# Performance work log

Hardware: AMD Instinct MI355X
Metric: run time of the kernel (lower is better)

The kernel has to match this reference:

```python
import jax, jax.numpy as jnp
import numpy as np

H = 51  # hidden size hard-coded in the module

def _lstm_cell(x_t, h, c, W_ih, W_hh, b_ih, b_hh):
    # PyTorch LSTMCell gate order: i, f, g, o
    gates = x_t @ W_ih.T + b_ih + h @ W_hh.T + b_hh  # [B, 4H]
    i, f, g, o = jnp.split(gates, 4, axis=-1)
    c_new = jax.nn.sigmoid(f) * c + jax.nn.sigmoid(i) * jnp.tanh(g)
    h_new = jax.nn.sigmoid(o) * jnp.tanh(c_new)
    return h_new, c_new


def setup_inputs() -> dict:
    key = jax.random.key(0)
    ks = jax.random.split(key, 11)
    B, T = 4096, 1024
    s = 1.0 / np.sqrt(H)
    return {
        "x": jax.random.normal(ks[0], (B, T), jnp.float32),
        "W_ih1": jax.random.uniform(ks[1], (4 * H, 1), jnp.float32, -s, s),
        "W_hh1": jax.random.uniform(ks[2], (4 * H, H), jnp.float32, -s, s),
        "b_ih1": jax.random.uniform(ks[3], (4 * H,), jnp.float32, -s, s),
        "b_hh1": jax.random.uniform(ks[4], (4 * H,), jnp.float32, -s, s),
        "W_ih2": jax.random.uniform(ks[5], (4 * H, H), jnp.float32, -s, s),
        "W_hh2": jax.random.uniform(ks[6], (4 * H, H), jnp.float32, -s, s),
        "b_ih2": jax.random.uniform(ks[7], (4 * H,), jnp.float32, -s, s),
        "b_hh2": jax.random.uniform(ks[8], (4 * H,), jnp.float32, -s, s),
        "W_lin": jax.random.uniform(ks[9], (1, H), jnp.float32, -s, s),
        "b_lin": jax.random.uniform(ks[10], (1,), jnp.float32, -s, s),
        "future": 64,
    }


def reference(x, W_ih1, W_hh1, b_ih1, b_hh1, W_ih2, W_hh2, b_ih2, b_hh2, W_lin, b_lin, future):
    B = x.shape[0]
    zeros = jnp.zeros((B, H), x.dtype)

    def step(carry, x_t):
        h1, c1, h2, c2 = carry
        h1, c1 = _lstm_cell(x_t, h1, c1, W_ih1, W_hh1, b_ih1, b_hh1)
        h2, c2 = _lstm_cell(h1, h2, c2, W_ih2, W_hh2, b_ih2, b_hh2)
        out = h2 @ W_lin.T + b_lin  # [B, 1]
        return (h1, c1, h2, c2), out

    xs = x.T[:, :, None]  # [T, B, 1]
    carry, outs = jax.lax.scan(step, (zeros, zeros, zeros, zeros), xs)

    def fut_step(carry, _):
        (h1, c1, h2, c2), out = carry
        h1, c1 = _lstm_cell(out, h1, c1, W_ih1, W_hh1, b_ih1, b_hh1)
        h2, c2 = _lstm_cell(h1, h2, c2, W_ih2, W_hh2, b_ih2, b_hh2)
        out = h2 @ W_lin.T + b_lin
        return ((h1, c1, h2, c2), out), out

    if future > 0:
        last_out = outs[-1]
        _, fut_outs = jax.lax.scan(fut_step, (carry, last_out), None, length=future)
        outs = jnp.concatenate([outs, fut_outs], axis=0)  # [T+future, B, 1]

    return outs[:, :, 0].T  # [B, T+future]
```

## Files before the change

kernel.cpp:

```cpp
#include <hip/hip_runtime.h>

#define HH    51
#define T_SEQ 1024
#define T_TOT 1088
#define B_TOT 4096
#define MT    16
#define NTH   512

typedef __attribute__((ext_vector_type(8))) short bf8_t;
typedef __attribute__((ext_vector_type(4))) float f32x4;

#define H1H_O 0
#define H1L_O 4096
#define H2H_O 8192
#define H2L_O 12288
#define XB_O  16384
#define OB_O  18432
#define PT_O  20480
#define SM_SZ 20992

#define L2E 1.44269504088896f

#if __has_builtin(__builtin_amdgcn_exp2f)
#define FEXP2 __builtin_amdgcn_exp2f
#else
#define FEXP2 exp2f
#endif
#if __has_builtin(__builtin_amdgcn_rcpf)
#define FRCP __builtin_amdgcn_rcpf
#else
#define FRCP(v) (1.f / (v))
#endif

__device__ __forceinline__ short f2bf(float f) {
  unsigned u = __builtin_bit_cast(unsigned, f);
  u += 0x7fffu + ((u >> 16) & 1u);
  return (short)(u >> 16);
}
__device__ __forceinline__ float bf2f(short s) {
  unsigned u = ((unsigned)(unsigned short)s) << 16;
  return __builtin_bit_cast(float, u);
}
__device__ __forceinline__ float lsig(float v) { return FRCP(1.f + FEXP2(v)); }

__device__ __forceinline__ f32x4 MFMA(bf8_t a, bf8_t b, f32x4 c) {
  return __builtin_amdgcn_mfma_f32_16x16x32_bf16(a, b, c, 0, 0, 0);
}
__device__ __forceinline__ bf8_t ldA(const char* base, int row, int off) {
  off ^= ((row & 7) << 4);
  return *reinterpret_cast<const bf8_t*>(base + row * 128 + off);
}
__device__ __forceinline__ void sthl(char* WH, char* WL, int row, int boff, float v) {
  const int o = row * 128 + (boff ^ ((row & 7) << 4));
  const unsigned u = __builtin_bit_cast(unsigned, v);
  *reinterpret_cast<short*>(WH + o) = (short)(u >> 16);
  const float rem = v - __builtin_bit_cast(float, u & 0xffff0000u);
  *reinterpret_cast<short*>(WL + o) = (short)(__builtin_bit_cast(unsigned, rem) >> 16);
}

__global__ __launch_bounds__(NTH, 1)
void lstm_mfma_kernel(const float* __restrict__ x,
                      const float* __restrict__ Wih1, const float* __restrict__ Whh1,
                      const float* __restrict__ bih1, const float* __restrict__ bhh1,
                      const float* __restrict__ Wih2, const float* __restrict__ Whh2,
                      const float* __restrict__ bih2, const float* __restrict__ bhh2,
                      const float* __restrict__ Wlin, const float* __restrict__ blin,
                      float* __restrict__ out)
{
  extern __shared__ char smc[];
  float* smf = (float*)smc;
  const int tid  = threadIdx.x;
  const int lane = tid & 63;
  const int w    = tid >> 6;
  const int cl   = lane & 15;
  const int gr   = lane >> 4;
  const int rng  = w & 3;
  const bool isL2 = (w >= 4);
  const int jo   = rng * 16 + cl;
  const bool jv  = (jo < HH);
  const int bg0  = blockIdx.x * MT;

  for (int i = tid; i < SM_SZ / 4; i += NTH) smf[i] = 0.f;

  const float gsc[4] = {-L2E, -L2E, 2.f * L2E, -L2E};

  bf8_t Bh[4][4], Bl[4][4];
  #pragma unroll
  for (int g = 0; g < 4; ++g) {
    #pragma unroll
    for (int kb = 0; kb < 4; ++kb) {
      bf8_t vh, vl;
      const bool dead = (!isL2 && kb >= 2);
      const float* Wsrc = isL2 ? (kb < 2 ? Wih2 : Whh2) : Whh1;
      const int kbase = (kb & 1) * 32;
      #pragma unroll
      for (int s = 0; s < 8; ++s) {
        const int ku = kbase + gr * 8 + s;
        float v = (!dead && jv && ku < HH) ? Wsrc[(g * HH + jo) * HH + ku] * gsc[g] : 0.f;
        if (!isL2 && kb == 1 && ku == 53) v = jv ? Wih1[g * HH + jo] * gsc[g] : 0.f;
        const short hh = f2bf(v);
        vh[s] = hh;
        vl[s] = f2bf(v - bf2f(hh));
      }
      Bh[g][kb] = vh; Bl[g][kb] = vl;
    }
  }
  bf8_t Bo[2];
  #pragma unroll
  for (int kb = 0; kb < 2; ++kb) {
    bf8_t v;
    #pragma unroll
    for (int s = 0; s < 8; ++s) {
      const int ku = kb * 32 + gr * 8 + s;
      float wv = (ku < HH) ? Wlin[ku] : 0.f;
      const short hh = f2bf(wv);
      v[s] = (cl == 0) ? hh : (cl == 1) ? f2bf(wv - bf2f(hh)) : (short)0;
    }
    Bo[kb] = v;
  }
  float cbv[4], wih1v[4];
  #pragma unroll
  for (int g = 0; g < 4; ++g) {
    cbv[g]   = jv ? (isL2 ? (bih2[g*HH+jo] + bhh2[g*HH+jo])
                          : (bih1[g*HH+jo] + bhh1[g*HH+jo])) * gsc[g] : 0.f;
    wih1v[g] = (jv && !isL2) ? Wih1[g*HH+jo] * gsc[g] : 0.f;
  }
  const float wlv = (jv && isL2) ? Wlin[jo] : 0.f;
  const float bl  = blin[0];
  float cst[4] = {0.f, 0.f, 0.f, 0.f};

  auto act_h = [&](const f32x4 acc[4], int r) -> float {
    const float si = lsig(acc[0][r]);
    const float sf = lsig(acc[1][r]);
    const float tg = 1.f - 2.f * lsig(acc[2][r]);
    const float so = lsig(acc[3][r]);
    const float cn = sf * cst[r] + si * tg;
    cst[r] = cn;
    return so * (1.f - 2.f * lsig(cn * (2.f * L2E)));
  };

  auto writeOB = [&](int tw, const float ov[4]) {
    if (cl == 0) {
      const int po = (tw >> 4) & 1, cc = tw & 15;
      #pragma unroll
      for (int r = 0; r < 4; ++r)
        smf[OB_O/4 + po*256 + (gr*4 + r)*16 + cc] = ov[r];
    }
  };

  auto do_l1 = [&](const int p, const float* xv, const int t) {
    const char* RH = smc + H1H_O + (p ^ 1) * 2048;
    const char* RL = smc + H1L_O + (p ^ 1) * 2048;
    bf8_t a0 = ldA(RH, cl, gr*16), a1 = ldA(RH, cl, 64 + gr*16);
    bf8_t l0 = ldA(RL, cl, gr*16), l1 = ldA(RL, cl, 64 + gr*16);
    f32x4 acc[4];
    __builtin_amdgcn_s_setprio(1);
    #pragma unroll
    for (int g = 0; g < 4; ++g) {
      f32x4 a = {cbv[g], cbv[g], cbv[g], cbv[g]};
      a = MFMA(a0, Bh[g][0], a); a = MFMA(a1, Bh[g][1], a);
      a = MFMA(l0, Bh[g][0], a); a = MFMA(l1, Bh[g][1], a);
      a = MFMA(a0, Bl[g][0], a); a = MFMA(a1, Bl[g][1], a);
      acc[g] = a;
    }
    __builtin_amdgcn_s_setprio(0);
    if (xv) {
      #pragma unroll
      for (int g = 0; g < 4; ++g)
        #pragma unroll
        for (int r = 0; r < 4; ++r) acc[g][r] += wih1v[g] * xv[r];
    }
    char* WH = smc + H1H_O + p * 2048;
    char* WL = smc + H1L_O + p * 2048;
    #pragma unroll
    for (int r = 0; r < 4; ++r) {
      const float hv = act_h(acc, r);
      if (jv) sthl(WH, WL, gr * 4 + r, 2 * jo, hv);
    }
    if (!xv && rng == 3 && (t + 1) < T_SEQ) {
      if (lane < 16) {
        const float xn = smf[XB_O/4 + (((t+1) >> 4) & 1) * 256 + lane * 16 + ((t+1) & 15)];
        sthl(WH, WL, lane, 2 * 53, xn);
      }
    }
  };

  auto do_l2 = [&](const int q, const bool ar, const int tw) {
    const char* R1H = smc + H1H_O + q * 2048,       *R1L = smc + H1L_O + q * 2048;
    const char* R2H = smc + H2H_O + (q ^ 1) * 2048, *R2L = smc + H2L_O + (q ^ 1) * 2048;
    bf8_t a[4], al[4];
    a[0]  = ldA(R1H, cl, gr*16); a[1]  = ldA(R1H, cl, 64 + gr*16);
    a[2]  = ldA(R2H, cl, gr*16); a[3]  = ldA(R2H, cl, 64 + gr*16);
    al[0] = ldA(R1L, cl, gr*16); al[1] = ldA(R1L, cl, 64 + gr*16);
    al[2] = ldA(R2L, cl, gr*16); al[3] = ldA(R2L, cl, 64 + gr*16);
    f32x4 acc[4];
    f32x4 d = {0.f, 0.f, 0.f, 0.f};
    __builtin_amdgcn_s_setprio(1);
    #pragma unroll
    for (int g = 0; g < 4; ++g) {
      f32x4 ac = {cbv[g], cbv[g], cbv[g], cbv[g]};
      #pragma unroll
      for (int kb = 0; kb < 4; ++kb) ac = MFMA(a[kb],  Bh[g][kb], ac);
      #pragma unroll
      for (int kb = 0; kb < 4; ++kb) ac = MFMA(al[kb], Bh[g][kb], ac);
      #pragma unroll
      for (int kb = 0; kb < 4; ++kb) ac = MFMA(a[kb],  Bl[g][kb], ac);
      acc[g] = ac;
    }
    if (!ar && rng == 0) {
      d = MFMA(a[3], Bo[1], d); d = MFMA(a[2], Bo[0], d);
      d = MFMA(al[3], Bo[1], d); d = MFMA(al[2], Bo[0], d);
    }
    __builtin_amdgcn_s_setprio(0);
    char* WH = smc + H2H_O + q * 2048;
    char* WL = smc + H2L_O + q * 2048;
    float po[4];
    #pragma unroll
    for (int r = 0; r < 4; ++r) {
      const float hv = act_h(acc, r);
      if (jv) sthl(WH, WL, gr * 4 + r, 2 * jo, hv);
      po[r] = wlv * hv;
    }
    if (!ar) {
      if (rng == 0 && tw >= 0) {
        float ov[4];
        #pragma unroll
        for (int r = 0; r < 4; ++r) ov[r] = d[r] + __shfl_xor(d[r], 1, 64) + bl;
        writeOB(tw, ov);
      }
    } else {
      #pragma unroll
      for (int r = 0; r < 4; ++r) {
        #pragma unroll
        for (int m = 1; m < 16; m <<= 1) po[r] += __shfl_xor(po[r], m, 64);
      }
      if (cl == 0) {
        #pragma unroll
        for (int r = 0; r < 4; ++r)
          smf[PT_O/4 + q*64 + rng*16 + gr*4 + r] = po[r];
      }
    }
  };

  auto finalize = [&](const int q, float ov[4]) {
    #pragma unroll
    for (int r = 0; r < 4; ++r) {
      const int row = gr * 4 + r;
      ov[r] = smf[PT_O/4 + q*64 +  0 + row] + smf[PT_O/4 + q*64 + 16 + row]
            + smf[PT_O/4 + q*64 + 32 + row] + smf[PT_O/4 + q*64 + 48 + row] + bl;
    }
  };
  auto flushOB = [&](int tb) {
    const int q = (tb >> 4) & 1;
    #pragma unroll
    for (int it = 0; it < 4; ++it) {
      const int idx = lane + 64 * it;
      const int r = idx >> 4, tt = idx & 15;
      out[(size_t)(bg0 + r) * T_TOT + tb + tt] = smf[OB_O/4 + q*256 + r*16 + tt];
    }
  };

  __syncthreads();
  if (tid < 256) {
    const int r = tid >> 4, tt = tid & 15;
    smf[XB_O/4 + r*16 + tt] = x[(size_t)(bg0 + r) * T_SEQ + tt];
  }
  if (tid < 16)
    sthl(smc + H1H_O + 2048, smc + H1L_O + 2048, tid, 2 * 53,
         x[(size_t)(bg0 + tid) * T_SEQ]);
  __syncthreads();

  auto main_step = [&](int t, const int p) {
    if (!isL2) {
      if ((w == 1 || w == 2) && (t & 15) == 0 && (t + 16) < T_SEQ) {
        const int nt = t + 16, par = (nt >> 4) & 1;
        #pragma unroll
        for (int it = 0; it < 2; ++it) {
          const int idx = (w - 1) * 128 + lane + 64 * it;
          const int r = idx >> 4, tt = idx & 15;
          smf[XB_O/4 + par*256 + r*16 + tt] = x[(size_t)(bg0 + r) * T_SEQ + nt + tt];
        }
      }
      if (w == 3 && (t & 15) == 9 && t >= 25) flushOB(((t - 2) & ~15) - 16);
      do_l1(p, nullptr, t);
    } else {
      if (t >= 1) do_l2(p ^ 1, false, t - 2);
    }
  };

  #pragma unroll 1
  for (int t = 0; t < T_SEQ; t += 2) {
    main_step(t, 0);
    __syncthreads();
    main_step(t + 1, 1);
    __syncthreads();
  }
  if (isL2) {
    do_l2(1, true, -1);
    if (rng == 0) {
      const char* RH = smc + H2H_O;
      const char* RL = smc + H2L_O;
      bf8_t a2 = ldA(RH, cl, gr*16), a3 = ldA(RH, cl, 64 + gr*16);
      bf8_t b2 = ldA(RL, cl, gr*16), b3 = ldA(RL, cl, 64 + gr*16);
      f32x4 d = {0.f, 0.f, 0.f, 0.f};
      d = MFMA(a3, Bo[1], d); d = MFMA(a2, Bo[0], d);
      d = MFMA(b3, Bo[1], d); d = MFMA(b2, Bo[0], d);
      float ov[4];
      #pragma unroll
      for (int r = 0; r < 4; ++r) ov[r] = d[r] + __shfl_xor(d[r], 1, 64) + bl;
      writeOB(1022, ov);
    }
  } else if (w == 3 && lane < 16) {
    sthl(smc + H1H_O,        smc + H1L_O,        lane, 2 * 53, 0.f);
    sthl(smc + H1H_O + 2048, smc + H1L_O + 2048, lane, 2 * 53, 0.f);
  }
  __syncthreads();

  auto ar_step = [&](int t, const int p) {
    if (!isL2) {
      float ov[4];
      finalize(p ^ 1, ov);
      if (w == 0) writeOB(t - 1, ov);
      if (w == 3 && (t & 15) == 8) flushOB(((t - 1) & ~15) - 16);
      do_l1(p, ov, t);
    }
    __syncthreads();
    if (isL2) do_l2(p, true, -1);
    __syncthreads();
  };
  #pragma unroll 1
  for (int t = T_SEQ; t < T_TOT; t += 2) {
    ar_step(t, 0);
    ar_step(t + 1, 1);
  }
  if (!isL2 && w == 0) { float ov[4]; finalize(1, ov); writeOB(T_TOT - 1, ov); }
  __syncthreads();
  if (w == 3) flushOB(T_TOT - 16);
}

extern "C" void kernel_launch(void* const* d_in, const int* in_sizes, int n_in,
                              void* d_out, int out_size, void* d_ws, size_t ws_size,
                              hipStream_t stream) {
  const float* x    = (const float*)d_in[0];
  const float* Wih1 = (const float*)d_in[1];
  const float* Whh1 = (const float*)d_in[2];
  const float* bih1 = (const float*)d_in[3];
  const float* bhh1 = (const float*)d_in[4];
  const float* Wih2 = (const float*)d_in[5];
  const float* Whh2 = (const float*)d_in[6];
  const float* bih2 = (const float*)d_in[7];
  const float* bhh2 = (const float*)d_in[8];
  const float* Wlin = (const float*)d_in[9];
  const float* blin = (const float*)d_in[10];
  float* out = (float*)d_out;

  lstm_mfma_kernel<<<B_TOT / MT, NTH, SM_SZ, stream>>>(
      x, Wih1, Whh1, bih1, bhh1, Wih2, Whh2, bih2, bhh2, Wlin, blin, out);
}
```

Baseline: 1.293 ms.

## Preload layer-1 hidden state for layer 2 and split MFMA accumulation chains

Layer-2 warps now read the freshly written h1 fragments from shared memory right after the barrier and keep them in registers for the next step, which shifts the layer-2 pipeline by one more step. Each gate's MFMA chain is also split into two independent accumulators that are summed at the end, shortening the dependent MFMA latency chain. The drain and epilogue logic are reworked to match the new schedule. This costs extra registers and adds more complex buffer-index bookkeeping.

```diff
diff --git a/kernel.cpp b/kernel.cpp
--- a/kernel.cpp
+++ b/kernel.cpp
@@ -148,20 +148,30 @@
     }
   };
 
-  auto do_l1 = [&](const int p, const float* xv, const int t) {
-    const char* RH = smc + H1H_O + (p ^ 1) * 2048;
-    const char* RL = smc + H1L_O + (p ^ 1) * 2048;
+  bf8_t pa0, pa1, pl0, pl1;
+  auto l2_preload = [&](const int hb) {
+    const char* RH = smc + H1H_O + hb * 2048;
+    const char* RL = smc + H1L_O + hb * 2048;
+    pa0 = ldA(RH, cl, gr*16); pa1 = ldA(RH, cl, 64 + gr*16);
+    pl0 = ldA(RL, cl, gr*16); pl1 = ldA(RL, cl, 64 + gr*16);
+  };
+
+  auto do_l1 = [&](const int rb, const int wb, const float* xv,
+                   const bool seedx, const int t) {
+    const char* RH = smc + H1H_O + rb * 2048;
+    const char* RL = smc + H1L_O + rb * 2048;
     bf8_t a0 = ldA(RH, cl, gr*16), a1 = ldA(RH, cl, 64 + gr*16);
     bf8_t l0 = ldA(RL, cl, gr*16), l1 = ldA(RL, cl, 64 + gr*16);
     f32x4 acc[4];
     __builtin_amdgcn_s_setprio(1);
     #pragma unroll
     for (int g = 0; g < 4; ++g) {
-      f32x4 a = {cbv[g], cbv[g], cbv[g], cbv[g]};
-      a = MFMA(a0, Bh[g][0], a); a = MFMA(a1, Bh[g][1], a);
-      a = MFMA(l0, Bh[g][0], a); a = MFMA(l1, Bh[g][1], a);
-      a = MFMA(a0, Bl[g][0], a); a = MFMA(a1, Bl[g][1], a);
-      acc[g] = a;
+      f32x4 aa = {cbv[g], cbv[g], cbv[g], cbv[g]};
+      aa = MFMA(a0, Bh[g][0], aa); aa = MFMA(a1, Bh[g][1], aa); aa = MFMA(l0, Bh[g][0], aa);
+      f32x4 ab = {0.f, 0.f, 0.f, 0.f};
+      ab = MFMA(l1, Bh[g][1], ab); ab = MFMA(a0, Bl[g][0], ab); ab = MFMA(a1, Bl[g][1], ab);
+      #pragma unroll
+      for (int r2 = 0; r2 < 4; ++r2) acc[g][r2] = aa[r2] + ab[r2];
     }
     __builtin_amdgcn_s_setprio(0);
     if (xv) {
@@ -170,50 +180,55 @@
         #pragma unroll
         for (int r = 0; r < 4; ++r) acc[g][r] += wih1v[g] * xv[r];
     }
-    char* WH = smc + H1H_O + p * 2048;
-    char* WL = smc + H1L_O + p * 2048;
+    char* WH = smc + H1H_O + wb * 2048;
+    char* WL = smc + H1L_O + wb * 2048;
     #pragma unroll
     for (int r = 0; r < 4; ++r) {
       const float hv = act_h(acc, r);
       if (jv) sthl(WH, WL, gr * 4 + r, 2 * jo, hv);
     }
-    if (!xv && rng == 3 && (t + 1) < T_SEQ) {
-      if (lane < 16) {
-        const float xn = smf[XB_O/4 + (((t+1) >> 4) & 1) * 256 + lane * 16 + ((t+1) & 15)];
-        sthl(WH, WL, lane, 2 * 53, xn);
-      }
-    }
-  };
-
-  auto do_l2 = [&](const int q, const bool ar, const int tw) {
-    const char* R1H = smc + H1H_O + q * 2048,       *R1L = smc + H1L_O + q * 2048;
-    const char* R2H = smc + H2H_O + (q ^ 1) * 2048, *R2L = smc + H2L_O + (q ^ 1) * 2048;
-    bf8_t a[4], al[4];
-    a[0]  = ldA(R1H, cl, gr*16); a[1]  = ldA(R1H, cl, 64 + gr*16);
-    a[2]  = ldA(R2H, cl, gr*16); a[3]  = ldA(R2H, cl, 64 + gr*16);
-    al[0] = ldA(R1L, cl, gr*16); al[1] = ldA(R1L, cl, 64 + gr*16);
-    al[2] = ldA(R2L, cl, gr*16); al[3] = ldA(R2L, cl, 64 + gr*16);
+    if (seedx && rng == 3 && lane < 16) {
+      const float xn = smf[XB_O/4 + (((t+1) >> 4) & 1) * 256 + lane * 16 + ((t+1) & 15)];
+      sthl(WH, WL, lane, 2 * 53, xn);
+    }
+  };
+
+  auto do_l2 = [&](const int h1b, const int h2r, const int h2w,
+                   const bool wantPT, const int ptq, const int tw) {
+    bf8_t a0, a1, u0, u1;
+    if (h1b >= 0) {
+      const char* R1H = smc + H1H_O + h1b * 2048;
+      const char* R1L = smc + H1L_O + h1b * 2048;
+      a0 = ldA(R1H, cl, gr*16); a1 = ldA(R1H, cl, 64 + gr*16);
+      u0 = ldA(R1L, cl, gr*16); u1 = ldA(R1L, cl, 64 + gr*16);
+    } else { a0 = pa0; a1 = pa1; u0 = pl0; u1 = pl1; }
+    const char* R2H = smc + H2H_O + h2r * 2048;
+    const char* R2L = smc + H2L_O + h2r * 2048;
+    bf8_t b0 = ldA(R2H, cl, gr*16), b1 = ldA(R2H, cl, 64 + gr*16);
+    bf8_t v0 = ldA(R2L, cl, gr*16), v1 = ldA(R2L, cl, 64 + gr*16);
     f32x4 acc[4];
     f32x4 d = {0.f, 0.f, 0.f, 0.f};
     __builtin_amdgcn_s_setprio(1);
     #pragma unroll
     for (int g = 0; g < 4; ++g) {
-      f32x4 ac = {cbv[g], cbv[g], cbv[g], cbv[g]};
-      #pragma unroll
-      for (int kb = 0; kb < 4; ++kb) ac = MFMA(a[kb],  Bh[g][kb], ac);
-      #pragma unroll
-      for (int kb = 0; kb < 4; ++kb) ac = MFMA(al[kb], Bh[g][kb], ac);
-      #pragma unroll
-      for (int kb = 0; kb < 4; ++kb) ac = MFMA(a[kb],  Bl[g][kb], ac);
-      acc[g] = ac;
-    }
-    if (!ar && rng == 0) {
-      d = MFMA(a[3], Bo[1], d); d = MFMA(a[2], Bo[0], d);
-      d = MFMA(al[3], Bo[1], d); d = MFMA(al[2], Bo[0], d);
+      f32x4 aa = {cbv[g], cbv[g], cbv[g], cbv[g]};
+      aa = MFMA(a0, Bh[g][0], aa); aa = MFMA(a1, Bh[g][1], aa);
+      aa = MFMA(u0, Bh[g][0], aa); aa = MFMA(u1, Bh[g][1], aa);
+      aa = MFMA(a0, Bl[g][0], aa); aa = MFMA(a1, Bl[g][1], aa);
+      f32x4 ab = {0.f, 0.f, 0.f, 0.f};
+      ab = MFMA(b0, Bh[g][2], ab); ab = MFMA(b1, Bh[g][3], ab);
+      ab = MFMA(v0, Bh[g][2], ab); ab = MFMA(v1, Bh[g][3], ab);
+      ab = MFMA(b0, Bl[g][2], ab); ab = MFMA(b1, Bl[g][3], ab);
+      #pragma unroll
+      for (int r2 = 0; r2 < 4; ++r2) acc[g][r2] = aa[r2] + ab[r2];
+    }
+    if (tw >= 0 && rng == 0) {
+      d = MFMA(b1, Bo[1], d); d = MFMA(b0, Bo[0], d);
+      d = MFMA(v1, Bo[1], d); d = MFMA(v0, Bo[0], d);
     }
     __builtin_amdgcn_s_setprio(0);
-    char* WH = smc + H2H_O + q * 2048;
-    char* WL = smc + H2L_O + q * 2048;
+    char* WH = smc + H2H_O + h2w * 2048;
+    char* WL = smc + H2L_O + h2w * 2048;
     float po[4];
     #pragma unroll
     for (int r = 0; r < 4; ++r) {
@@ -221,14 +236,13 @@
       if (jv) sthl(WH, WL, gr * 4 + r, 2 * jo, hv);
       po[r] = wlv * hv;
     }
-    if (!ar) {
-      if (rng == 0 && tw >= 0) {
-        float ov[4];
-        #pragma unroll
-        for (int r = 0; r < 4; ++r) ov[r] = d[r] + __shfl_xor(d[r], 1, 64) + bl;
-        writeOB(tw, ov);
-      }
-    } else {
+    if (tw >= 0 && rng == 0) {
+      float ov[4];
+      #pragma unroll
+      for (int r = 0; r < 4; ++r) ov[r] = d[r] + __shfl_xor(d[r], 1, 64) + bl;
+      writeOB(tw, ov);
+    }
+    if (wantPT) {
       #pragma unroll
       for (int r = 0; r < 4; ++r) {
         #pragma unroll
@@ -237,7 +251,7 @@
       if (cl == 0) {
         #pragma unroll
         for (int r = 0; r < 4; ++r)
-          smf[PT_O/4 + q*64 + rng*16 + gr*4 + r] = po[r];
+          smf[PT_O/4 + ptq*64 + rng*16 + gr*4 + r] = po[r];
       }
     }
   };
@@ -270,50 +284,49 @@
          x[(size_t)(bg0 + tid) * T_SEQ]);
   __syncthreads();
 
-  auto main_step = [&](int t, const int p) {
-    if (!isL2) {
-      if ((w == 1 || w == 2) && (t & 15) == 0 && (t + 16) < T_SEQ) {
-        const int nt = t + 16, par = (nt >> 4) & 1;
-        #pragma unroll
-        for (int it = 0; it < 2; ++it) {
-          const int idx = (w - 1) * 128 + lane + 64 * it;
-          const int r = idx >> 4, tt = idx & 15;
-          smf[XB_O/4 + par*256 + r*16 + tt] = x[(size_t)(bg0 + r) * T_SEQ + nt + tt];
+  #pragma unroll 1
+  for (int t2 = 0; t2 < T_SEQ; t2 += 2) {
+    {
+      const int t = t2;
+      if (!isL2) {
+        if ((w == 1 || w == 2) && (t & 15) == 0 && (t + 16) < T_SEQ) {
+          const int nt = t + 16, par = (nt >> 4) & 1;
+          #pragma unroll
+          for (int it = 0; it < 2; ++it) {
+            const int idx = (w - 1) * 128 + lane + 64 * it;
+            const int r = idx >> 4, tt = idx & 15;
+            smf[XB_O/4 + par*256 + r*16 + tt] = x[(size_t)(bg0 + r) * T_SEQ + nt + tt];
+          }
         }
-      }
-      if (w == 3 && (t & 15) == 9 && t >= 25) flushOB(((t - 2) & ~15) - 16);
-      do_l1(p, nullptr, t);
-    } else {
-      if (t >= 1) do_l2(p ^ 1, false, t - 2);
-    }
-  };
-
-  #pragma unroll 1
-  for (int t = 0; t < T_SEQ; t += 2) {
-    main_step(t, 0);
-    __syncthreads();
-    main_step(t + 1, 1);
-    __syncthreads();
-  }
+        do_l1(1, 0, nullptr, true, t);
+      } else {
+        if (t >= 2) do_l2(-1, 1, 0, false, 0, t - 3);
+        if (t >= 1) l2_preload(1);
+      }
+      __syncthreads();
+    }
+    {
+      const int t = t2 + 1;
+      if (!isL2) {
+        if (w == 3 && (t & 15) == 9 && t >= 25) flushOB(((t - 2) & ~15) - 16);
+        do_l1(0, 1, nullptr, (t + 1) < T_SEQ, t);
+      } else {
+        if (t >= 2) do_l2(-1, 0, 1, false, 0, t - 3);
+        l2_preload(0);
+      }
+      __syncthreads();
+    }
+  }
+
   if (isL2) {
-    do_l2(1, true, -1);
-    if (rng == 0) {
-      const char* RH = smc + H2H_O;
-      const char* RL = smc + H2L_O;
-      bf8_t a2 = ldA(RH, cl, gr*16), a3 = ldA(RH, cl, 64 + gr*16);
-      bf8_t b2 = ldA(RL, cl, gr*16), b3 = ldA(RL, cl, 64 + gr*16);
-      f32x4 d = {0.f, 0.f, 0.f, 0.f};
-      d = MFMA(a3, Bo[1], d); d = MFMA(a2, Bo[0], d);
-      d = MFMA(b3, Bo[1], d); d = MFMA(b2, Bo[0], d);
-      float ov[4];
-      #pragma unroll
-      for (int r = 0; r < 4; ++r) ov[r] = d[r] + __shfl_xor(d[r], 1, 64) + bl;
-      writeOB(1022, ov);
-    }
+    do_l2(-1, 1, 0, false, 0, 1021);
+    l2_preload(1);
   } else if (w == 3 && lane < 16) {
     sthl(smc + H1H_O,        smc + H1L_O,        lane, 2 * 53, 0.f);
     sthl(smc + H1H_O + 2048, smc + H1L_O + 2048, lane, 2 * 53, 0.f);
   }
+  __syncthreads();
+  if (isL2) do_l2(-1, 0, 1, true, 1, 1022);
   __syncthreads();
 
   auto ar_step = [&](int t, const int p) {
@@ -322,10 +335,10 @@
       finalize(p ^ 1, ov);
       if (w == 0) writeOB(t - 1, ov);
       if (w == 3 && (t & 15) == 8) flushOB(((t - 1) & ~15) - 16);
-      do_l1(p, ov, t);
+      do_l1(p ^ 1, p, ov, false, t);
     }
     __syncthreads();
-    if (isL2) do_l2(p, true, -1);
+    if (isL2) do_l2(p, p ^ 1, p, true, p, -1);
     __syncthreads();
   };
   #pragma unroll 1
```

Result: slower. 1.369 ms (+5.9%).
